# Kernel optimization log

Hardware: AMD Instinct MI355X
Metric: run time of the kernel (lower is better)

The kernel has to match this reference:

```python
import jax, jax.numpy as jnp
import numpy as np

MAX_RADIUS = 3.0
NUM_BASIS = 8
NUM_NEIGHBORS = 16.0
N, E, NS, NV, B, D, T, L, HR = 2048, 32768, 32, 16, 8, 32, 32, 2, 64
NW = NS * 2 * NV + NV * 2 * (NS + NV) + NV * 2 * NV  # 3072 per-edge TP weights


def smooth_cutoff(x):
    u = 2.0 * (x - 1.0)
    y = 0.5 * (1.0 - jnp.cos(jnp.pi * u))
    y = jnp.where(u > 0, 0.0, y)
    y = jnp.where(u < -1, 1.0, y)
    return y


def bessel_basis(length):
    # soft_one_hot_linspace(basis='bessel', cutoff=False) * sqrt(NUM_BASIS)
    k = jnp.arange(1, NUM_BASIS + 1, dtype=length.dtype) * jnp.pi
    l = jnp.maximum(length, 1e-9)[..., None]
    return jnp.sqrt(2.0 / MAX_RADIUS) * jnp.sin(k * l / MAX_RADIUS) / l * np.sqrt(NUM_BASIS)


def get_edge_info(x, edge_src, edge_dst):
    n = x.shape[0]
    xr = x.reshape(n, 2, 3)                         # 2 vectors per node
    vec = xr[edge_src] - xr[edge_dst]               # [E,2,3]
    length = jnp.sqrt(jnp.sum(vec * vec, axis=-1) + 1e-12)   # [E,2]
    sh = np.sqrt(3.0) * vec / length[..., None]     # component-normalized l=1 SH
    feat = bessel_basis(length)                     # [E,2,B]
    attr = smooth_cutoff(length / MAX_RADIUS)[..., None] * sh  # [E,2,3]
    return feat.reshape(vec.shape[0], -1), attr


def setup_inputs() -> dict:
    key = jax.random.key(0)
    ks = jax.random.split(key, 20)
    inp = {
        'x': jax.random.normal(ks[0], (N, 6), jnp.float32),
        'batch': jnp.zeros((N,), jnp.int64 if jax.config.jax_enable_x64 else jnp.int32),
        'node_attr': jax.random.randint(ks[1], (N,), 0, T),
        'edge_src': jax.random.randint(ks[2], (E,), 0, N),
        'edge_dst': jax.random.randint(ks[3], (E,), 0, N),
        'emb': jax.random.normal(ks[4], (T, D), jnp.float32),
        'W_uplift': jax.random.normal(ks[5], (NV, 2), jnp.float32),
        'W_sc_s': jax.random.normal(ks[6], (L, NS, D, NS + NV), jnp.float32),
        'W_sc_v': jax.random.normal(ks[7], (L, NV, D, NV), jnp.float32),
        'W_l1_s': jax.random.normal(ks[8], (L, NS, NS), jnp.float32),
        'W_l1_v': jax.random.normal(ks[9], (L, NV, NV), jnp.float32),
        'W_r1': jax.random.normal(ks[10], (L, 2 * B, HR), jnp.float32),
        'W_r2': jax.random.normal(ks[11], (L, HR, NW), jnp.float32),
        'W_l2_s': jax.random.normal(ks[12], (L, NS + NV, NS + NV), jnp.float32),
        'W_l2_v': jax.random.normal(ks[13], (L, NV, NV), jnp.float32),
        'W_si_s': jax.random.normal(ks[14], (L, NS, NS), jnp.float32),
        'W_si_v': jax.random.normal(ks[15], (L, NV, NV), jnp.float32),
        'h': jnp.ones((L,), jnp.float32) * 0.01,
        'mix': jnp.ones((L,), jnp.float32) * 0.5,
    }
    return inp


def reference(x, batch, node_attr, edge_src, edge_dst, emb, W_uplift, W_sc_s, W_sc_v,
              W_l1_s, W_l1_v, W_r1, W_r2, W_l2_s, W_l2_v, W_si_s, W_si_v, h, mix):
    n = x.shape[0]
    a = emb[node_attr]                              # node attr embedding [N,D]
    Q, _ = jnp.linalg.qr(W_uplift)                  # semi-unitary uplift [NV,2]
    y_v = jnp.einsum('ci,nik->nck', Q, x.reshape(n, 2, 3))   # uplift vectors
    y_s = jnp.zeros((n, NS), x.dtype)
    y, y_old = (y_s, y_v), (y_s, y_v)
    n1 = NS * 2 * NV
    n2 = NV * 2 * (NS + NV)
    for i in range(L):
        ef, ea = get_edge_info(x, edge_src, edge_dst)       # [E,2B], [E,2,3]
        ys, yv = y
        # self-connection tensor product (features x node_attr)
        sc_s = jnp.einsum('ni,na,iaj->nj', ys, a, W_sc_s[i]) / np.sqrt(NS * D)
        sc_v = jnp.einsum('nck,na,caj->njk', yv, a, W_sc_v[i]) / np.sqrt(NV * D)
        # lin1
        s1 = ys @ W_l1_s[i] / np.sqrt(NS)
        v1 = jnp.einsum('nck,cj->njk', yv, W_l1_v[i]) / np.sqrt(NV)
        # radial MLP -> per-edge TP weights
        hr = jax.nn.silu(ef @ W_r1[i] / np.sqrt(2 * B))
        w = hr @ W_r2[i] / np.sqrt(HR)                       # [E,NW]
        w_sv = w[:, :n1].reshape(E, NS, 2, NV)
        w_vs = w[:, n1:n1 + n2].reshape(E, NV, 2, NS + NV)
        w_vv = w[:, n1 + n2:].reshape(E, NV, 2, NV)
        s_src, v_src = s1[edge_src], v1[edge_src]
        # edge tensor product: 0e x 1o -> 1o, 1o x 1o -> 0e (dot), 1o x 1o -> 1o (cross)
        e_v = jnp.einsum('esmj,es,emk->ejk', w_sv, s_src, ea) / np.sqrt(NS * 2)
        dots = jnp.einsum('eck,emk->ecm', v_src, ea)
        e_s = jnp.einsum('ecmj,ecm->ej', w_vs, dots) / np.sqrt(NV * 2 * 3)
        crs = jnp.cross(v_src[:, :, None, :], ea[:, None, :, :])  # [E,NV,2,3]
        e_v = e_v + jnp.einsum('ecmj,ecmk->ejk', w_vv, crs) / np.sqrt(NV * 2 * 2)
        # scatter-aggregate over destination nodes
        ns_ = jax.ops.segment_sum(e_s, edge_dst, num_segments=n) / np.sqrt(NUM_NEIGHBORS)
        nv_ = jax.ops.segment_sum(e_v, edge_dst, num_segments=n) / np.sqrt(NUM_NEIGHBORS)
        s2 = ns_ @ W_l2_s[i] / np.sqrt(NS + NV)
        v2 = jnp.einsum('nck,cj->njk', nv_, W_l2_v[i]) / np.sqrt(NV)
        conv_s, conv_v = sc_s + s2, sc_v + v2
        # gate
        g_s = jax.nn.silu(conv_s[:, :NS])
        g_v = jax.nn.sigmoid(conv_s[:, NS:])[:, :, None] * conv_v
        # self-interaction
        si_s = ys @ W_si_s[i] / np.sqrt(NS)
        si_v = jnp.einsum('nck,cj->njk', yv, W_si_v[i]) / np.sqrt(NV)
        # gated leapfrog update
        h2, m = h[i] ** 2, mix[i]
        new_s = 2 * ys - y_old[0] + h2 * (m * g_s + (m - 1) * si_s)
        new_v = 2 * yv - y_old[1] + h2 * (m * g_v + (m - 1) * si_v)
        y_old, y = y, (new_s, new_v)
        x = jnp.einsum('ci,nck->nik', Q, y[1]).reshape(n, 6)  # project back
    return x
```

## Files before the change

### kernel.cpp

```cpp
#include <hip/hip_runtime.h>
#include <hip/hip_bf16.h>
#include <math.h>

#define NN   2048
#define EE   32768
#define NS   32
#define NV   16
#define NB   8
#define DD   32
#define TT   32
#define LL   2
#define HRD  64
#define NWW  3072
#define TPE  128
#define PI_F 3.14159265358979323846f

#define SC_SCS (1.0f/32.0f)
#define SC_SCV 0.04419417382415922f
#define SC_L1S 0.17677669529663687f
#define SC_L1V 0.25f
#define SC_R1  0.25f
#define SC_R2  0.125f
#define SC_ES  0.10206207261596575f
#define SC_EV  0.125f
#define SC_AGG 0.25f
#define SC_L2S 0.14433756729740643f
#define SC_L2V 0.25f
#define SC_SIS 0.17677669529663687f
#define SC_SIV 0.25f

typedef __attribute__((ext_vector_type(8))) short  short8;
typedef __attribute__((ext_vector_type(4))) float  floatx4;

__device__ __forceinline__ floatx4 mfma16(short8 a, short8 b, floatx4 c) {
    return __builtin_amdgcn_mfma_f32_16x16x32_bf16(a, b, c, 0, 0, 0);
}

__device__ __forceinline__ void seg_reduce_store(
        const float (*red)[49], const int* dst_s,
        const int* __restrict__ row_ptr, int ebase,
        int tid, int wave, int lane,
        int* segstart_s, int* wtot_s, int* nseg_s,
        float* __restrict__ outg) {
    int seg_flag = 0, seg_lidx = 0;
    if (tid < TPE) {
        seg_flag = (tid == 0) || (dst_s[tid] != dst_s[tid - 1]);
        unsigned long long m = __ballot(seg_flag != 0);
        if (lane == 0) wtot_s[wave] = (int)__popcll(m);
        seg_lidx = (int)__popcll(m & ((1ull << lane) - 1ull));
    }
    __syncthreads();
    if (seg_flag) segstart_s[seg_lidx + (wave ? wtot_s[0] : 0)] = tid;
    if (tid == 0) {
        int ns = wtot_s[0] + wtot_s[1];
        nseg_s[0] = ns;
        segstart_s[ns] = TPE;
    }
    __syncthreads();
    int nseg = nseg_s[0];
    for (int w = tid; w < nseg * 48; w += 256) {
        int seg = w / 48, c = w - seg * 48;
        int p0 = segstart_s[seg], p1 = segstart_s[seg + 1];
        int d = dst_s[p0];
        float run = 0.f;
        for (int pos = p0; pos < p1; ++pos) run += red[pos][c];
        if (row_ptr[d] >= ebase && row_ptr[d + 1] <= ebase + TPE)
            outg[d * 48 + c] = run;
        else
            atomicAdd(&outg[d * 48 + c], run);
    }
}

__global__ void k_setup(const float* __restrict__ Wup, float* __restrict__ Q,
                        const float* __restrict__ emb,
                        const float* __restrict__ Wscs, const float* __restrict__ Wscv,
                        float* __restrict__ WtS, float* __restrict__ WtV,
                        const float* __restrict__ Wr2, __hip_bfloat16* __restrict__ wr2t,
                        int* __restrict__ deg, int* __restrict__ cursor) {
    int b = blockIdx.x;
    if (b == 0) {
        if (threadIdx.x != 0) return;
        double A[16][2], tau[2];
        for (int i = 0; i < 16; ++i)
            for (int j = 0; j < 2; ++j) A[i][j] = (double)Wup[i*2 + j];
        for (int j = 0; j < 2; ++j) {
            double alpha = A[j][j];
            double xn2 = 0.0;
            for (int i = j + 1; i < 16; ++i) xn2 += A[i][j]*A[i][j];
            if (xn2 == 0.0) {
                tau[j] = 0.0;
            } else {
                double nrm  = sqrt(alpha*alpha + xn2);
                double beta = (alpha >= 0.0) ? -nrm : nrm;
                tau[j] = (beta - alpha) / beta;
                double s = 1.0 / (alpha - beta);
                for (int i = j + 1; i < 16; ++i) A[i][j] *= s;
                A[j][j] = beta;
            }
            for (int k = j + 1; k < 2; ++k) {
                double w = A[j][k];
                for (int i = j + 1; i < 16; ++i) w += A[i][j]*A[i][k];
                w *= tau[j];
                A[j][k] -= w;
                for (int i = j + 1; i < 16; ++i) A[i][k] -= A[i][j]*w;
            }
        }
        double Qm[16][2];
        for (int i = 0; i < 16; ++i)
            for (int j = 0; j < 2; ++j) Qm[i][j] = (i == j) ? 1.0 : 0.0;
        for (int j = 1; j >= 0; --j) {
            for (int k = 0; k < 2; ++k) {
                double w = Qm[j][k];
                for (int i = j + 1; i < 16; ++i) w += A[i][j]*Qm[i][k];
                w *= tau[j];
                Qm[j][k] -= w;
                for (int i = j + 1; i < 16; ++i) Qm[i][k] -= A[i][j]*w;
            }
        }
        for (int i = 0; i < 16; ++i)
            for (int j = 0; j < 2; ++j) Q[i*2 + j] = (float)Qm[i][j];
    } else if (b <= 64) {
        int lt = b - 1;
        int l = lt >> 5, t = lt & 31;
        __shared__ float es[32];
        if (threadIdx.x < 32) es[threadIdx.x] = emb[t*DD + threadIdx.x];
        __syncthreads();
        const float* Ws = Wscs + (size_t)l*NS*DD*48;
        float* oS = WtS + (size_t)(l*TT + t)*NS*48;
        for (int idx = threadIdx.x; idx < NS*48; idx += 256) {
            int i = idx / 48, j = idx % 48;
            float acc = 0.f;
            for (int a = 0; a < 32; ++a) acc += es[a]*Ws[(i*DD + a)*48 + j];
            oS[idx] = acc;
        }
        const float* Wv = Wscv + (size_t)l*NV*DD*NV;
        float* oV = WtV + (size_t)(l*TT + t)*NV*NV;
        for (int idx = threadIdx.x; idx < NV*NV; idx += 256) {
            int c = idx / 16, j = idx % 16;
            float acc = 0.f;
            for (int a = 0; a < 32; ++a) acc += es[a]*Wv[(c*DD + a)*NV + j];
            oV[idx] = acc;
        }
    } else if (b <= 1600) {
        int idx = (b - 65)*256 + threadIdx.x;
        int l = idx / (HRD*NWW);
        int r = idx - l*(HRD*NWW);
        int k = r / NWW;
        int c = r - k*NWW;
        int ch = c >> 6, cc = c & 63, q = cc >> 4, tcc = cc & 15;
        int h = k >> 5, qd = (k >> 3) & 3, j = k & 7;
        size_t dst = (size_t)l*(NWW*HRD)
                   + (size_t)((ch*32 + q*8 + h*4 + qd)*128 + tcc*8 + j);
        wr2t[dst] = __float2bfloat16(Wr2[idx]);
    } else {
        int i = (b - 1601)*256 + threadIdx.x;
        if (i < NN) { deg[i] = 0; cursor[i] = 0; }
    }
}

__global__ void k_hist(const int* __restrict__ edst, int* __restrict__ deg) {
    int e = blockIdx.x*256 + threadIdx.x;
    atomicAdd(&deg[edst[e]], 1);
}

__global__ void k_scan(const int* __restrict__ deg, int* __restrict__ row_ptr) {
    __shared__ int part[256];
    __shared__ int psc[256];
    int t = threadIdx.x;
    int loc[8]; int s = 0;
    for (int k = 0; k < 8; ++k) { loc[k] = deg[t*8 + k]; s += loc[k]; }
    part[t] = s;
    __syncthreads();
    if (t == 0) { int run = 0; for (int i = 0; i < 256; ++i) { psc[i] = run; run += part[i]; } }
    __syncthreads();
    int off = psc[t];
    for (int k = 0; k < 8; ++k) { row_ptr[t*8 + k] = off; off += loc[k]; }
    if (t == 255) row_ptr[2048] = off;
}

__global__ void k_fill(const int* __restrict__ esrc, const int* __restrict__ edst,
                       const int* __restrict__ row_ptr, int* __restrict__ cursor,
                       int* __restrict__ srcs, int* __restrict__ dsts,
                       const float* __restrict__ xin, const float* __restrict__ Q,
                       float* __restrict__ ys0, float* __restrict__ yv0,
                       float* __restrict__ ys1, float* __restrict__ yv1,
                       float* __restrict__ xcur,
                       const float* __restrict__ Wl1v0,
                       float* __restrict__ s1, float* __restrict__ v1,
                       float* __restrict__ nsb, float* __restrict__ nsb2,
                       float* __restrict__ nvba, float* __restrict__ nvbb) {
    if (blockIdx.x < 128) {
        int e = blockIdx.x*256 + threadIdx.x;
        int d = edst[e];
        int pos = atomicAdd(&cursor[d], 1);
        int p = row_ptr[d] + pos;
        srcs[p] = esrc[e];
        dsts[p] = d;
    } else {
        int idx = (blockIdx.x - 128)*256 + threadIdx.x;
        int n = idx / 48, r = idx - 48*(idx / 48);
        int j = r/3, k = r - 3*j;
        float xk  = xin[n*6 + k];
        float xk3 = xin[n*6 + 3 + k];
        float yvv = Q[j*2 + 0]*xk + Q[j*2 + 1]*xk3;
        yv0[idx] = yvv;
        yv1[idx] = yvv;
        float a = 0.f;
        for (int c = 0; c < 16; ++c) {
            float yc = Q[c*2 + 0]*xk + Q[c*2 + 1]*xk3;
            a += yc*Wl1v0[c*16 + j];
        }
        v1[idx] = a*SC_L1V;
        nsb[idx] = 0.f; nsb2[idx] = 0.f;
        nvba[idx] = 0.f; nvbb[idx] = 0.f;
        if (r < 32) {
            int si = n*32 + r;
            ys0[si] = 0.f; ys1[si] = 0.f; s1[si] = 0.f;
        }
        if (r < 6) xcur[n*6 + r] = xin[n*6 + r];
    }
}

__global__ void __launch_bounds__(256, 3) k_tp(
        const float* __restrict__ xcur,
        const int* __restrict__ srcs, const int* __restrict__ dsts,
        const int* __restrict__ row_ptr,
        const float* __restrict__ Wr1l,
        const __hip_bfloat16* __restrict__ wr2tl,
        const float* __restrict__ s1g, const float* __restrict__ v1g,
        float* __restrict__ nsb, float* __restrict__ nsb2,
        float* __restrict__ nvba, float* __restrict__ nvbb) {
    __shared__ __align__(16) char smem[42240];
    __shared__ float ea_s[TPE][9];
    __shared__ int   src_s[TPE];
    __shared__ int   dst_s[TPE];
    __shared__ int   segstart_s[TPE + 1];
    __shared__ int   wtot_s[2];
    __shared__ int   nseg_s[1];

    int bid = blockIdx.x;
    int region = bid % 3;
    int tile   = bid / 3;
    int ebase  = tile*TPE;
    int tid = threadIdx.x;
    int wave = tid >> 6, lane = tid & 63;
    int tc = tid & 15;
    int quad = lane >> 4;

    float* ef_lds  = (float*)smem;
    float* Wr1_lds = (float*)(smem + 8448);
    __hip_bfloat16* hr_lds = (__hip_bfloat16*)(smem + 12544);

    if (tid < TPE) { src_s[tid] = srcs[ebase + tid]; dst_s[tid] = dsts[ebase + tid]; }
    for (int i = tid; i < 16*64; i += 256) Wr1_lds[i] = Wr1l[i];

    if (tid < TPE) {
        int s = src_s[tid], d = dst_s[tid];
        for (int m = 0; m < 2; ++m) {
            float v0 = xcur[s*6 + m*3 + 0] - xcur[d*6 + m*3 + 0];
            float v1_ = xcur[s*6 + m*3 + 1] - xcur[d*6 + m*3 + 1];
            float v2 = xcur[s*6 + m*3 + 2] - xcur[d*6 + m*3 + 2];
            float len = sqrtf(v0*v0 + v1_*v1_ + v2*v2 + 1e-12f);
            float inv = 1.0f/len;
            float theta = len*(PI_F/3.0f);
            float s1v = sinf(theta), c1v = cosf(theta);
            float sc  = 2.3094010767585034f*inv;
            float sp = 0.f, scur = s1v, twoc = 2.f*c1v;
            for (int bq = 0; bq < 8; ++bq) {
                ef_lds[(m*8 + bq)*132 + tid] = sc*scur;
                float sn = twoc*scur - sp;
                sp = scur; scur = sn;
            }
            float u = 2.0f*(len*(1.0f/3.0f) - 1.0f);
            float cut;
            if (u > 0.f) cut = 0.f;
            else if (u < -1.f) cut = 1.f;
            else cut = 0.5f*(1.0f - cosf(PI_F*u));
            float shs = 1.7320508075688772f*inv*cut;
            ea_s[tid][m*3 + 0] = shs*v0;
            ea_s[tid][m*3 + 1] = shs*v1_;
            ea_s[tid][m*3 + 2] = shs*v2;
        }
    }
    __syncthreads();

    {
        int e = tid >> 1, h = tid & 1;
        float z[32];
        #pragma unroll
        for (int k = 0; k < 32; ++k) z[k] = 0.f;
        for (int f = 0; f < 16; ++f) {
            float efv = ef_lds[f*132 + e];
            #pragma unroll
            for (int k = 0; k < 32; ++k) z[k] += efv*Wr1_lds[f*64 + h*32 + k];
        }
        #pragma unroll
        for (int q8 = 0; q8 < 4; ++q8) {
            __hip_bfloat16 tmp[8];
            #pragma unroll
            for (int j = 0; j < 8; ++j) {
                float zz = z[q8*8 + j]*SC_R1;
                tmp[j] = __float2bfloat16(zz/(1.0f + expf(-zz)));
            }
            *(short8*)&hr_lds[e*72 + h*32 + q8*8] = *(short8*)tmp;
        }
    }
    __syncthreads();

    const short* hrp = (const short*)(smem + 12544);
    short8 a_lo[2], a_hi[2];
    #pragma unroll
    for (int rt = 0; rt < 2; ++rt) {
        int row = (wave*2 + rt)*16 + tc;
        a_lo[rt] = *(const short8*)(hrp + row*72 + quad*8);
        a_hi[rt] = *(const short8*)(hrp + row*72 + 32 + quad*8);
    }
    __syncthreads();

    const char* wb = (const char*)wr2tl;
    const float sES = SC_R2*SC_ES*SC_AGG;
    const float sEV = SC_R2*SC_EV*SC_AGG;

    if (region == 0) {
        float (*s1t)[132] = (float(*)[132])smem;
        for (int i = tid; i < TPE*32; i += 256) {
            int e = i >> 5, s = i & 31;
            s1t[s][e] = s1g[src_s[e]*32 + s];
        }
        __syncthreads();

        float accF[2][4][2] = {};
        for (int ci = 0; ci < 16; ++ci) {
            const char* Bc = wb + (size_t)ci*8192 + lane*16;
            #pragma unroll
            for (int q = 0; q < 4; ++q) {
                short8 b_lo = *(const short8*)(Bc + q*2048);
                short8 b_hi = *(const short8*)(Bc + q*2048 + 1024);
                floatx4 c0 = {0.f,0.f,0.f,0.f}, c1 = {0.f,0.f,0.f,0.f};
                c0 = mfma16(a_lo[0], b_lo, c0); c0 = mfma16(a_hi[0], b_hi, c0);
                c1 = mfma16(a_lo[1], b_lo, c1); c1 = mfma16(a_hi[1], b_hi, c1);
                int m = q & 1;
                int sidx = ci*2 + (q >> 1);
                #pragma unroll
                for (int rt = 0; rt < 2; ++rt) {
                    int e0r = (wave*2 + rt)*16 + quad*4;
                    float4 sv = *(const float4*)&s1t[sidx][e0r];
                    floatx4 cc = rt ? c1 : c0;
                    #pragma unroll
                    for (int i = 0; i < 4; ++i)
                        accF[rt][i][m] += cc[i]*((&sv.x)[i]);
                }
            }
        }
        __syncthreads();
        float (*red)[49] = (float(*)[49])smem;
        #pragma unroll
        for (int rt = 0; rt < 2; ++rt) {
            int e0r = (wave*2 + rt)*16 + quad*4;
            #pragma unroll
            for (int i = 0; i < 4; ++i) {
                int pos = e0r + i;
                float f0 = accF[rt][i][0]*sEV, f1 = accF[rt][i][1]*sEV;
                #pragma unroll
                for (int k = 0; k < 3; ++k)
                    red[pos][tc*3 + k] = f0*ea_s[pos][k] + f1*ea_s[pos][3 + k];
            }
        }
        __syncthreads();
        seg_reduce_store((const float(*)[49])smem, dst_s, row_ptr, ebase,
                         tid, wave, lane, segstart_s, wtot_s, nseg_s, nvba);
    } else if (region == 1) {
        float (*dots_t)[132] = (float(*)[132])smem;
        float (*v1t)[132]    = (float(*)[132])(smem + 16896);
        for (int i = tid; i < TPE*48; i += 256) {
            int e = i/48, j = i%48;
            v1t[j][e] = v1g[src_s[e]*48 + j];
        }
        __syncthreads();
        for (int i = tid; i < TPE*32; i += 256) {
            int cm = i >> 7, e = i & (TPE - 1), c = cm >> 1, m = cm & 1;
            dots_t[cm][e] = v1t[c*3+0][e]*ea_s[e][m*3+0]
                          + v1t[c*3+1][e]*ea_s[e][m*3+1]
                          + v1t[c*3+2][e]*ea_s[e][m*3+2];
        }
        __syncthreads();

        float accES[2][4][3] = {};
        for (int ci = 16; ci < 32; ++ci) {
            const char* Bc = wb + (size_t)ci*8192 + lane*16;
            #pragma unroll
            for (int q = 0; q < 4; ++q) {
                short8 b_lo = *(const short8*)(Bc + q*2048);
                short8 b_hi = *(const short8*)(Bc + q*2048 + 1024);
                floatx4 c0 = {0.f,0.f,0.f,0.f}, c1 = {0.f,0.f,0.f,0.f};
                c0 = mfma16(a_lo[0], b_lo, c0); c0 = mfma16(a_hi[0], b_hi, c0);
                c1 = mfma16(a_lo[1], b_lo, c1); c1 = mfma16(a_hi[1], b_hi, c1);
                int u = ci*4 + q - 64;
                int c = (u*10923) >> 16;
                int v6 = u - 6*c;
                int m = (v6 >= 3) ? 1 : 0;
                int g = v6 - 3*m;
                #pragma unroll
                for (int rt = 0; rt < 2; ++rt) {
                    int e0r = (wave*2 + rt)*16 + quad*4;
                    float4 dv = *(const float4*)&dots_t[c*2 + m][e0r];
                    floatx4 cc = rt ? c1 : c0;
                    #pragma unroll
                    for (int i = 0; i < 4; ++i)
                        accES[rt][i][g] += cc[i]*((&dv.x)[i]);
                }
            }
        }
        __syncthreads();
        float (*red)[49] = (float(*)[49])smem;
        #pragma unroll
        for (int rt = 0; rt < 2; ++rt) {
            int e0r = (wave*2 + rt)*16 + quad*4;
            #pragma unroll
            for (int i = 0; i < 4; ++i) {
                int pos = e0r + i;
                red[pos][tc]      = accES[rt][i][0]*sES;
                red[pos][16 + tc] = accES[rt][i][1]*sES;
                red[pos][32 + tc] = accES[rt][i][2]*sES;
            }
        }
        __syncthreads();
        seg_reduce_store((const float(*)[49])smem, dst_s, row_ptr, ebase,
                         tid, wave, lane, segstart_s, wtot_s, nseg_s, nsb);
    } else {
        float (*v1t)[132]  = (float(*)[132])smem;
        float (*dots2)[132] = (float(*)[132])(smem + 25344);
        for (int i = tid; i < TPE*48; i += 256) {
            int e = i/48, j = i%48;
            v1t[j][e] = v1g[src_s[e]*48 + j];
        }
        __syncthreads();
        for (int i = tid; i < 12*TPE; i += 256) {
            int r = i >> 7, e = i & (TPE - 1);
            int c = 10 + (r >> 1), m = r & 1;
            dots2[r][e] = v1t[c*3+0][e]*ea_s[e][m*3+0]
                        + v1t[c*3+1][e]*ea_s[e][m*3+1]
                        + v1t[c*3+2][e]*ea_s[e][m*3+2];
        }
        __syncthreads();

        float accES[2][4][3] = {};
        float accV[2][4][2][3] = {};
        for (int ci = 32; ci < 48; ++ci) {
            const char* Bc = wb + (size_t)ci*8192 + lane*16;
            #pragma unroll
            for (int q = 0; q < 4; ++q) {
                short8 b_lo = *(const short8*)(Bc + q*2048);
                short8 b_hi = *(const short8*)(Bc + q*2048 + 1024);
                floatx4 c0 = {0.f,0.f,0.f,0.f}, c1 = {0.f,0.f,0.f,0.f};
                c0 = mfma16(a_lo[0], b_lo, c0); c0 = mfma16(a_hi[0], b_hi, c0);
                c1 = mfma16(a_lo[1], b_lo, c1); c1 = mfma16(a_hi[1], b_hi, c1);
                if (ci < 40) {
                    int u = ci*4 + q - 64;
                    int c = (u*10923) >> 16;
                    int v6 = u - 6*c;
                    int m = (v6 >= 3) ? 1 : 0;
                    int g = v6 - 3*m;
                    int dr = (c - 10)*2 + m;
                    #pragma unroll
                    for (int rt = 0; rt < 2; ++rt) {
                        int e0r = (wave*2 + rt)*16 + quad*4;
                        float4 dv = *(const float4*)&dots2[dr][e0r];
                        floatx4 cc = rt ? c1 : c0;
                        #pragma unroll
                        for (int i = 0; i < 4; ++i)
                            accES[rt][i][g] += cc[i]*((&dv.x)[i]);
                    }
                } else {
                    int c = ci*2 - 80 + (q >> 1);
                    int m = q & 1;
                    #pragma unroll
                    for (int rt = 0; rt < 2; ++rt) {
                        int e0r = (wave*2 + rt)*16 + quad*4;
                        float4 vx = *(const float4*)&v1t[c*3 + 0][e0r];
                        float4 vy = *(const float4*)&v1t[c*3 + 1][e0r];
                        float4 vz = *(const float4*)&v1t[c*3 + 2][e0r];
                        floatx4 cc = rt ? c1 : c0;
                        #pragma unroll
                        for (int i = 0; i < 4; ++i) {
                            float ww = cc[i];
                            accV[rt][i][m][0] += ww*((&vx.x)[i]);
                            accV[rt][i][m][1] += ww*((&vy.x)[i]);
                            accV[rt][i][m][2] += ww*((&vz.x)[i]);
                        }
                    }
                }
            }
        }
        __syncthreads();
        float (*red)[49] = (float(*)[49])smem;
        #pragma unroll
        for (int rt = 0; rt < 2; ++rt) {
            int e0r = (wave*2 + rt)*16 + quad*4;
            #pragma unroll
            for (int i = 0; i < 4; ++i) {
                int pos = e0r + i;
                red[pos][tc]      = accES[rt][i][0]*sES;
                red[pos][16 + tc] = accES[rt][i][1]*sES;
                red[pos][32 + tc] = accES[rt][i][2]*sES;
            }
        }
        __syncthreads();
        seg_reduce_store((const float(*)[49])smem, dst_s, row_ptr, ebase,
                         tid, wave, lane, segstart_s, wtot_s, nseg_s, nsb2);
        __syncthreads();
        #pragma unroll
        for (int rt = 0; rt < 2; ++rt) {
            int e0r = (wave*2 + rt)*16 + quad*4;
            #pragma unroll
            for (int i = 0; i < 4; ++i) {
                int pos = e0r + i;
                float u00 = accV[rt][i][0][0], u01 = accV[rt][i][0][1], u02 = accV[rt][i][0][2];
                float u10 = accV[rt][i][1][0], u11 = accV[rt][i][1][1], u12 = accV[rt][i][1][2];
                float a0 = ea_s[pos][0], a1 = ea_s[pos][1], a2 = ea_s[pos][2];
                float b0 = ea_s[pos][3], b1 = ea_s[pos][4], b2 = ea_s[pos][5];
                red[pos][tc*3 + 0] = (u01*a2 - u02*a1 + u11*b2 - u12*b1)*sEV;
                red[pos][tc*3 + 1] = (u02*a0 - u00*a2 + u12*b0 - u10*b2)*sEV;
                red[pos][tc*3 + 2] = (u00*a1 - u01*a0 + u10*b1 - u11*b0)*sEV;
            }
        }
        __syncthreads();
        seg_reduce_store((const float(*)[49])smem, dst_s, row_ptr, ebase,
                         tid, wave, lane, segstart_s, wtot_s, nseg_s, nvbb);
    }
}

__global__ void __launch_bounds__(256) k_nodepost(
        const float* __restrict__ ysC, const float* __restrict__ yvC,
        float* __restrict__ ysO, float* __restrict__ yvO,
        const float* __restrict__ nsb, const float* __restrict__ nsb2,
        const float* __restrict__ nvba, const float* __restrict__ nvbb,
        const int* __restrict__ nattr,
        const float* __restrict__ WtSl, const float* __restrict__ WtVl,
        const float* __restrict__ Wl2s, const float* __restrict__ Wl2v,
        const float* __restrict__ Wsis, const float* __restrict__ Wsiv,
        const float* __restrict__ harr, const float* __restrict__ mixarr, int l,
        float* __restrict__ xcur, float* __restrict__ xout2,
        const float* __restrict__ Qg,
        const float* __restrict__ Wl1sN, const float* __restrict__ Wl1vN,
        float* __restrict__ s1, float* __restrict__ v1,
        float* __restrict__ znsb, float* __restrict__ znsb2,
        float* __restrict__ znvba, float* __restrict__ znvbb,
        int do_next) {
    int wave = threadIdx.x >> 6, lane = threadIdx.x & 63;
    int n = blockIdx.x*4 + wave;
    __shared__ float ys_s[4][32], yv_s[4][48], ns_s[4][48], nv_s[4][48];
    __shared__ float cs_s[4][48], nvo_s[4][48], nsn_s[4][32];

    if (lane < 32) ys_s[wave][lane] = ysC[n*32 + lane];
    if (lane < 48) {
        yv_s[wave][lane] = yvC[n*48 + lane];
        ns_s[wave][lane] = nsb[n*48 + lane] + nsb2[n*48 + lane];
        nv_s[wave][lane] = nvba[n*48 + lane] + nvbb[n*48 + lane];
    }
    __syncthreads();
    int t = nattr[n];
    const float* WtSn = WtSl + (size_t)t*NS*48;
    const float* WtVn = WtVl + (size_t)t*NV*NV;
    float hv = harr[l];
    float h2 = hv*hv, mx = mixarr[l];

    if (lane < 48) {
        float sc = 0.f, s2 = 0.f;
        for (int i = 0; i < 32; ++i) sc += ys_s[wave][i]*WtSn[i*48 + lane];
        for (int c = 0; c < 48; ++c) s2 += ns_s[wave][c]*Wl2s[c*48 + lane];
        cs_s[wave][lane] = sc*SC_SCS + s2*SC_L2S;
    }
    __syncthreads();
    if (lane < 48) {
        int j = lane/3, k = lane - 3*j;
        float scv = 0.f, v2 = 0.f, siv = 0.f;
        for (int c = 0; c < 16; ++c) {
            float yvv = yv_s[wave][c*3 + k];
            scv += yvv*WtVn[c*16 + j];
            v2  += nv_s[wave][c*3 + k]*Wl2v[c*16 + j];
            siv += yvv*Wsiv[c*16 + j];
        }
        float convv = scv*SC_SCV + v2*SC_L2V;
        siv *= SC_SIV;
        float gate = 1.f/(1.f + expf(-cs_s[wave][32 + j]));
        float gv = gate*convv;
        float nvnew = 2.f*yv_s[wave][lane] - yvO[n*48 + lane] + h2*(mx*gv + (mx - 1.f)*siv);
        nvo_s[wave][lane] = nvnew;
        yvO[n*48 + lane] = nvnew;
    }
    if (lane < 32) {
        float sis = 0.f;
        for (int i = 0; i < 32; ++i) sis += ys_s[wave][i]*Wsis[i*32 + lane];
        sis *= SC_SIS;
        float cs = cs_s[wave][lane];
        float gs = cs/(1.f + expf(-cs));
        float nsnew = 2.f*ys_s[wave][lane] - ysO[n*32 + lane] + h2*(mx*gs + (mx - 1.f)*sis);
        nsn_s[wave][lane] = nsnew;
        ysO[n*32 + lane] = nsnew;
    }
    __syncthreads();
    if (lane < 6) {
        int i = lane/3, k = lane - 3*(lane/3);
        float acc = 0.f;
        for (int c = 0; c < 16; ++c) acc += Qg[c*2 + i]*nvo_s[wave][c*3 + k];
        xcur[n*6 + lane]  = acc;
        xout2[n*6 + lane] = acc;
    }
    if (do_next) {
        if (lane < 32) {
            float a = 0.f;
            for (int i = 0; i < 32; ++i) a += nsn_s[wave][i]*Wl1sN[i*32 + lane];
            s1[n*32 + lane] = a*SC_L1S;
        }
        if (lane < 48) {
            int j = lane/3, k = lane - 3*j;
            float a = 0.f;
            for (int c = 0; c < 16; ++c) a += nvo_s[wave][c*3 + k]*Wl1vN[c*16 + j];
            v1[n*48 + lane] = a*SC_L1V;
            znsb[n*48 + lane] = 0.f; znsb2[n*48 + lane] = 0.f;
            znvba[n*48 + lane] = 0.f; znvbb[n*48 + lane] = 0.f;
        }
    }
}

extern "C" void kernel_launch(void* const* d_in, const int* in_sizes, int n_in,
                              void* d_out, int out_size, void* d_ws, size_t ws_size,
                              hipStream_t stream) {
    const float* x_in  = (const float*)d_in[0];
    const int*   nattr = (const int*)  d_in[2];
    const int*   esrc  = (const int*)  d_in[3];
    const int*   edst  = (const int*)  d_in[4];
    const float* emb   = (const float*)d_in[5];
    const float* Wup   = (const float*)d_in[6];
    const float* Wscs  = (const float*)d_in[7];
    const float* Wscv  = (const float*)d_in[8];
    const float* Wl1s  = (const float*)d_in[9];
    const float* Wl1v  = (const float*)d_in[10];
    const float* Wr1   = (const float*)d_in[11];
    const float* Wr2   = (const float*)d_in[12];
    const float* Wl2s  = (const float*)d_in[13];
    const float* Wl2v  = (const float*)d_in[14];
    const float* Wsis  = (const float*)d_in[15];
    const float* Wsiv  = (const float*)d_in[16];
    const float* harr  = (const float*)d_in[17];
    const float* mixar = (const float*)d_in[18];
    float* out = (float*)d_out;

    float* ws = (float*)d_ws;
    size_t off = 0;
    float* Q    = ws + off; off += 32;
    float* WtS  = ws + off; off += (size_t)LL*TT*NS*48;
    float* WtV  = ws + off; off += (size_t)LL*TT*NV*NV;
    float* ys0  = ws + off; off += (size_t)NN*32;
    float* yv0  = ws + off; off += (size_t)NN*48;
    float* ys1  = ws + off; off += (size_t)NN*32;
    float* yv1  = ws + off; off += (size_t)NN*48;
    float* xcur = ws + off; off += (size_t)NN*6;
    float* s1   = ws + off; off += (size_t)NN*32;
    float* v1   = ws + off; off += (size_t)NN*48;
    float* nsb  = ws + off; off += (size_t)NN*48;
    float* nsb2 = ws + off; off += (size_t)NN*48;
    float* nvba = ws + off; off += (size_t)NN*48;
    float* nvbb = ws + off; off += (size_t)NN*48;
    off = (off + 3) & ~(size_t)3;
    __hip_bfloat16* wr2t = (__hip_bfloat16*)(ws + off); off += (size_t)LL*NWW*HRD/2;
    int* deg     = (int*)(ws + off); off += NN;
    int* cursor  = (int*)(ws + off); off += NN;
    int* row_ptr = (int*)(ws + off); off += NN + 1;
    int* srcs    = (int*)(ws + off); off += EE;
    int* dsts    = (int*)(ws + off); off += EE;

    k_setup<<<1609, 256, 0, stream>>>(Wup, Q, emb, Wscs, Wscv, WtS, WtV, Wr2, wr2t,
                                      deg, cursor);
    k_hist<<<EE/256, 256, 0, stream>>>(edst, deg);
    k_scan<<<1, 256, 0, stream>>>(deg, row_ptr);
    k_fill<<<128 + NN*48/256, 256, 0, stream>>>(esrc, edst, row_ptr, cursor, srcs, dsts,
                                    x_in, Q, ys0, yv0, ys1, yv1, xcur,
                                    Wl1v, s1, v1, nsb, nsb2, nvba, nvbb);

    float* curS = ys0; float* curV = yv0;
    float* oldS = ys1; float* oldV = yv1;
    for (int l = 0; l < LL; ++l) {
        k_tp<<<3*EE/TPE, 256, 0, stream>>>(xcur, srcs, dsts, row_ptr,
                                           Wr1 + (size_t)l*16*64,
                                           wr2t + (size_t)l*NWW*HRD,
                                           s1, v1, nsb, nsb2, nvba, nvbb);
        float* xo2 = (l == LL - 1) ? out : xcur;
        int lN = (l + 1 < LL) ? (l + 1) : l;
        k_nodepost<<<NN/4, 256, 0, stream>>>(curS, curV, oldS, oldV,
                                             nsb, nsb2, nvba, nvbb, nattr,
                                             WtS + (size_t)l*TT*NS*48, WtV + (size_t)l*TT*NV*NV,
                                             Wl2s + (size_t)l*48*48, Wl2v + (size_t)l*16*16,
                                             Wsis + (size_t)l*32*32, Wsiv + (size_t)l*16*16,
                                             harr, mixar, l, xcur, xo2, Q,
                                             Wl1s + (size_t)lN*32*32, Wl1v + (size_t)lN*16*16,
                                             s1, v1, nsb, nsb2, nvba, nvbb,
                                             (l + 1 < LL) ? 1 : 0);
        float* ts = curS; curS = oldS; oldS = ts;
        float* tv = curV; curV = oldV; oldV = tv;
    }
}
```

Before: 232.4 us.

## Shrink tensor-product LDS footprint to raise occupancy; warp-shuffle scan for CSR

The region-1 staging of gathered v1 values now runs in two halves of 24 columns, which cuts the shared scratch buffer from 42240 to 31680 bytes. The launch bound is raised from 3 to 4 blocks per CU so more blocks can be resident and hide gather latency. This adds an extra round of barriers and may force register spilling under the tighter register budget. Separately, the single-thread serial prefix over 256 partial sums is replaced by a wavefront shuffle scan plus a small cross-wave combine.

```diff
diff --git a/kernel.cpp b/kernel.cpp
--- a/kernel.cpp
+++ b/kernel.cpp
@@ -164,16 +164,21 @@
 }
 
 __global__ void k_scan(const int* __restrict__ deg, int* __restrict__ row_ptr) {
-    __shared__ int part[256];
-    __shared__ int psc[256];
+    __shared__ int wsum[4];
     int t = threadIdx.x;
+    int lane = t & 63, wave = t >> 6;
     int loc[8]; int s = 0;
     for (int k = 0; k < 8; ++k) { loc[k] = deg[t*8 + k]; s += loc[k]; }
-    part[t] = s;
-    __syncthreads();
-    if (t == 0) { int run = 0; for (int i = 0; i < 256; ++i) { psc[i] = run; run += part[i]; } }
-    __syncthreads();
-    int off = psc[t];
+    int inc = s;
+    for (int d = 1; d < 64; d <<= 1) {
+        int v = __shfl_up(inc, d);
+        if (lane >= d) inc += v;
+    }
+    if (lane == 63) wsum[wave] = inc;
+    __syncthreads();
+    int woff = 0;
+    for (int w = 0; w < wave; ++w) woff += wsum[w];
+    int off = woff + inc - s;
     for (int k = 0; k < 8; ++k) { row_ptr[t*8 + k] = off; off += loc[k]; }
     if (t == 255) row_ptr[2048] = off;
 }
@@ -221,7 +226,7 @@
     }
 }
 
-__global__ void __launch_bounds__(256, 3) k_tp(
+__global__ void __launch_bounds__(256, 4) k_tp(
         const float* __restrict__ xcur,
         const int* __restrict__ srcs, const int* __restrict__ dsts,
         const int* __restrict__ row_ptr,
@@ -230,7 +235,7 @@
         const float* __restrict__ s1g, const float* __restrict__ v1g,
         float* __restrict__ nsb, float* __restrict__ nsb2,
         float* __restrict__ nvba, float* __restrict__ nvbb) {
-    __shared__ __align__(16) char smem[42240];
+    __shared__ __align__(16) char smem[31680];
     __shared__ float ea_s[TPE][9];
     __shared__ int   src_s[TPE];
     __shared__ int   dst_s[TPE];
@@ -371,19 +376,23 @@
                          tid, wave, lane, segstart_s, wtot_s, nseg_s, nvba);
     } else if (region == 1) {
         float (*dots_t)[132] = (float(*)[132])smem;
-        float (*v1t)[132]    = (float(*)[132])(smem + 16896);
-        for (int i = tid; i < TPE*48; i += 256) {
-            int e = i/48, j = i%48;
-            v1t[j][e] = v1g[src_s[e]*48 + j];
-        }
-        __syncthreads();
-        for (int i = tid; i < TPE*32; i += 256) {
-            int cm = i >> 7, e = i & (TPE - 1), c = cm >> 1, m = cm & 1;
-            dots_t[cm][e] = v1t[c*3+0][e]*ea_s[e][m*3+0]
-                          + v1t[c*3+1][e]*ea_s[e][m*3+1]
-                          + v1t[c*3+2][e]*ea_s[e][m*3+2];
-        }
-        __syncthreads();
+        float (*v1h)[132]    = (float(*)[132])(smem + 16896);
+        for (int half = 0; half < 2; ++half) {
+            int jbase = half*24;
+            for (int i = tid; i < TPE*24; i += 256) {
+                int e = i/24, j = i - 24*(i/24);
+                v1h[j][e] = v1g[src_s[e]*48 + jbase + j];
+            }
+            __syncthreads();
+            for (int i = tid; i < TPE*16; i += 256) {
+                int cm = i >> 7, e = i & (TPE - 1);
+                int c = cm >> 1, m = cm & 1;
+                dots_t[half*16 + cm][e] = v1h[c*3+0][e]*ea_s[e][m*3+0]
+                                        + v1h[c*3+1][e]*ea_s[e][m*3+1]
+                                        + v1h[c*3+2][e]*ea_s[e][m*3+2];
+            }
+            __syncthreads();
+        }
 
         float accES[2][4][3] = {};
         for (int ci = 16; ci < 32; ++ci) {
```

Result: slower. 281.1 us (+21.0%).

## Halve edge tile to 64 per block and use wave-shuffle scan

Applied to the files above, without the earlier changes.

Shrinks the per-block edge tile in the tensor-product kernel from 128 to 64 edges. That doubles the grid and halves LDS use, and each wave now handles one 16-row MFMA tile instead of two. The segment reduction drops to a single-wave ballot, and the prefix-scan kernel swaps its serial thread-0 loop for a shuffle-based wave scan. The aim is more blocks and occupancy to hide latency, at the cost of reloading the bf16 weight B-fragments from global memory twice as often and doing more boundary atomics.

```diff
diff --git a/kernel.cpp b/kernel.cpp
--- a/kernel.cpp
+++ b/kernel.cpp
@@ -12,7 +12,7 @@
 #define LL   2
 #define HRD  64
 #define NWW  3072
-#define TPE  128
+#define TPE  64
 #define PI_F 3.14159265358979323846f
 
 #define SC_SCS (1.0f/32.0f)
@@ -39,22 +39,20 @@
 __device__ __forceinline__ void seg_reduce_store(
         const float (*red)[49], const int* dst_s,
         const int* __restrict__ row_ptr, int ebase,
-        int tid, int wave, int lane,
+        int tid, int lane,
         int* segstart_s, int* wtot_s, int* nseg_s,
         float* __restrict__ outg) {
-    int seg_flag = 0, seg_lidx = 0;
     if (tid < TPE) {
-        seg_flag = (tid == 0) || (dst_s[tid] != dst_s[tid - 1]);
+        int seg_flag = (tid == 0) || (dst_s[tid] != dst_s[tid - 1]);
         unsigned long long m = __ballot(seg_flag != 0);
-        if (lane == 0) wtot_s[wave] = (int)__popcll(m);
-        seg_lidx = (int)__popcll(m & ((1ull << lane) - 1ull));
-    }
-    __syncthreads();
-    if (seg_flag) segstart_s[seg_lidx + (wave ? wtot_s[0] : 0)] = tid;
+        if (lane == 0) wtot_s[0] = (int)__popcll(m);
+        int seg_lidx = (int)__popcll(m & ((1ull << lane) - 1ull));
+        if (seg_flag) segstart_s[seg_lidx] = tid;
+    }
+    __syncthreads();
     if (tid == 0) {
-        int ns = wtot_s[0] + wtot_s[1];
-        nseg_s[0] = ns;
-        segstart_s[ns] = TPE;
+        nseg_s[0] = wtot_s[0];
+        segstart_s[wtot_s[0]] = TPE;
     }
     __syncthreads();
     int nseg = nseg_s[0];
@@ -164,16 +162,21 @@
 }
 
 __global__ void k_scan(const int* __restrict__ deg, int* __restrict__ row_ptr) {
-    __shared__ int part[256];
-    __shared__ int psc[256];
+    __shared__ int wsum[4];
     int t = threadIdx.x;
+    int lane = t & 63, wave = t >> 6;
     int loc[8]; int s = 0;
     for (int k = 0; k < 8; ++k) { loc[k] = deg[t*8 + k]; s += loc[k]; }
-    part[t] = s;
-    __syncthreads();
-    if (t == 0) { int run = 0; for (int i = 0; i < 256; ++i) { psc[i] = run; run += part[i]; } }
-    __syncthreads();
-    int off = psc[t];
+    int inc = s;
+    for (int d = 1; d < 64; d <<= 1) {
+        int v = __shfl_up(inc, d);
+        if (lane >= d) inc += v;
+    }
+    if (lane == 63) wsum[wave] = inc;
+    __syncthreads();
+    int woff = 0;
+    for (int w = 0; w < wave; ++w) woff += wsum[w];
+    int off = woff + inc - s;
     for (int k = 0; k < 8; ++k) { row_ptr[t*8 + k] = off; off += loc[k]; }
     if (t == 255) row_ptr[2048] = off;
 }
@@ -230,12 +233,12 @@
         const float* __restrict__ s1g, const float* __restrict__ v1g,
         float* __restrict__ nsb, float* __restrict__ nsb2,
         float* __restrict__ nvba, float* __restrict__ nvbb) {
-    __shared__ __align__(16) char smem[42240];
+    __shared__ __align__(16) char smem[21760];
     __shared__ float ea_s[TPE][9];
     __shared__ int   src_s[TPE];
     __shared__ int   dst_s[TPE];
     __shared__ int   segstart_s[TPE + 1];
-    __shared__ int   wtot_s[2];
+    __shared__ int   wtot_s[1];
     __shared__ int   nseg_s[1];
 
     int bid = blockIdx.x;
@@ -248,8 +251,8 @@
     int quad = lane >> 4;
 
     float* ef_lds  = (float*)smem;
-    float* Wr1_lds = (float*)(smem + 8448);
-    __hip_bfloat16* hr_lds = (__hip_bfloat16*)(smem + 12544);
+    float* Wr1_lds = (float*)(smem + 4352);
+    __hip_bfloat16* hr_lds = (__hip_bfloat16*)(smem + 8448);
 
     if (tid < TPE) { src_s[tid] = srcs[ebase + tid]; dst_s[tid] = dsts[ebase + tid]; }
     for (int i = tid; i < 16*64; i += 256) Wr1_lds[i] = Wr1l[i];
@@ -267,7 +270,7 @@
             float sc  = 2.3094010767585034f*inv;
             float sp = 0.f, scur = s1v, twoc = 2.f*c1v;
             for (int bq = 0; bq < 8; ++bq) {
-                ef_lds[(m*8 + bq)*132 + tid] = sc*scur;
+                ef_lds[(m*8 + bq)*68 + tid] = sc*scur;
                 float sn = twoc*scur - sp;
                 sp = scur; scur = sn;
             }
@@ -285,158 +288,135 @@
     __syncthreads();
 
     {
-        int e = tid >> 1, h = tid & 1;
-        float z[32];
+        int e = tid >> 2, h = tid & 3;
+        float z[16];
         #pragma unroll
-        for (int k = 0; k < 32; ++k) z[k] = 0.f;
+        for (int k = 0; k < 16; ++k) z[k] = 0.f;
         for (int f = 0; f < 16; ++f) {
-            float efv = ef_lds[f*132 + e];
+            float efv = ef_lds[f*68 + e];
             #pragma unroll
-            for (int k = 0; k < 32; ++k) z[k] += efv*Wr1_lds[f*64 + h*32 + k];
+            for (int k = 0; k < 16; ++k) z[k] += efv*Wr1_lds[f*64 + h*16 + k];
         }
         #pragma unroll
-        for (int q8 = 0; q8 < 4; ++q8) {
+        for (int q8 = 0; q8 < 2; ++q8) {
             __hip_bfloat16 tmp[8];
             #pragma unroll
             for (int j = 0; j < 8; ++j) {
                 float zz = z[q8*8 + j]*SC_R1;
                 tmp[j] = __float2bfloat16(zz/(1.0f + expf(-zz)));
             }
-            *(short8*)&hr_lds[e*72 + h*32 + q8*8] = *(short8*)tmp;
-        }
-    }
-    __syncthreads();
-
-    const short* hrp = (const short*)(smem + 12544);
-    short8 a_lo[2], a_hi[2];
-    #pragma unroll
-    for (int rt = 0; rt < 2; ++rt) {
-        int row = (wave*2 + rt)*16 + tc;
-        a_lo[rt] = *(const short8*)(hrp + row*72 + quad*8);
-        a_hi[rt] = *(const short8*)(hrp + row*72 + 32 + quad*8);
-    }
+            *(short8*)&hr_lds[e*72 + h*16 + q8*8] = *(short8*)tmp;
+        }
+    }
+    __syncthreads();
+
+    const short* hrp = (const short*)(smem + 8448);
+    int arow = wave*16 + tc;
+    short8 a_lo = *(const short8*)(hrp + arow*72 + quad*8);
+    short8 a_hi = *(const short8*)(hrp + arow*72 + 32 + quad*8);
     __syncthreads();
 
     const char* wb = (const char*)wr2tl;
     const float sES = SC_R2*SC_ES*SC_AGG;
     const float sEV = SC_R2*SC_EV*SC_AGG;
+    int e0r = wave*16 + quad*4;
 
     if (region == 0) {
-        float (*s1t)[132] = (float(*)[132])smem;
+        float (*s1t)[68] = (float(*)[68])smem;
         for (int i = tid; i < TPE*32; i += 256) {
             int e = i >> 5, s = i & 31;
             s1t[s][e] = s1g[src_s[e]*32 + s];
         }
         __syncthreads();
 
-        float accF[2][4][2] = {};
+        float accF[4][2] = {};
         for (int ci = 0; ci < 16; ++ci) {
             const char* Bc = wb + (size_t)ci*8192 + lane*16;
             #pragma unroll
             for (int q = 0; q < 4; ++q) {
                 short8 b_lo = *(const short8*)(Bc + q*2048);
                 short8 b_hi = *(const short8*)(Bc + q*2048 + 1024);
-                floatx4 c0 = {0.f,0.f,0.f,0.f}, c1 = {0.f,0.f,0.f,0.f};
-                c0 = mfma16(a_lo[0], b_lo, c0); c0 = mfma16(a_hi[0], b_hi, c0);
-                c1 = mfma16(a_lo[1], b_lo, c1); c1 = mfma16(a_hi[1], b_hi, c1);
+                floatx4 c0 = {0.f,0.f,0.f,0.f};
+                c0 = mfma16(a_lo, b_lo, c0); c0 = mfma16(a_hi, b_hi, c0);
                 int m = q & 1;
                 int sidx = ci*2 + (q >> 1);
+                float4 sv = *(const float4*)&s1t[sidx][e0r];
                 #pragma unroll
-                for (int rt = 0; rt < 2; ++rt) {
-                    int e0r = (wave*2 + rt)*16 + quad*4;
-                    float4 sv = *(const float4*)&s1t[sidx][e0r];
-                    floatx4 cc = rt ? c1 : c0;
-                    #pragma unroll
-                    for (int i = 0; i < 4; ++i)
-                        accF[rt][i][m] += cc[i]*((&sv.x)[i]);
-                }
+                for (int i = 0; i < 4; ++i)
+                    accF[i][m] += c0[i]*((&sv.x)[i]);
             }
         }
         __syncthreads();
         float (*red)[49] = (float(*)[49])smem;
         #pragma unroll
-        for (int rt = 0; rt < 2; ++rt) {
-            int e0r = (wave*2 + rt)*16 + quad*4;
+        for (int i = 0; i < 4; ++i) {
+            int pos = e0r + i;
+            float f0 = accF[i][0]*sEV, f1 = accF[i][1]*sEV;
             #pragma unroll
-            for (int i = 0; i < 4; ++i) {
-                int pos = e0r + i;
-                float f0 = accF[rt][i][0]*sEV, f1 = accF[rt][i][1]*sEV;
-                #pragma unroll
-                for (int k = 0; k < 3; ++k)
-                    red[pos][tc*3 + k] = f0*ea_s[pos][k] + f1*ea_s[pos][3 + k];
-            }
+            for (int k = 0; k < 3; ++k)
+                red[pos][tc*3 + k] = f0*ea_s[pos][k] + f1*ea_s[pos][3 + k];
         }
         __syncthreads();
         seg_reduce_store((const float(*)[49])smem, dst_s, row_ptr, ebase,
-                         tid, wave, lane, segstart_s, wtot_s, nseg_s, nvba);
+                         tid, lane, segstart_s, wtot_s, nseg_s, nvba);
     } else if (region == 1) {
-        float (*dots_t)[132] = (float(*)[132])smem;
-        float (*v1t)[132]    = (float(*)[132])(smem + 16896);
+        float (*dots_t)[68] = (float(*)[68])smem;
+        float (*v1t)[68]    = (float(*)[68])(smem + 8704);
         for (int i = tid; i < TPE*48; i += 256) {
-            int e = i/48, j = i%48;
+            int e = i/48, j = i - 48*(i/48);
             v1t[j][e] = v1g[src_s[e]*48 + j];
         }
         __syncthreads();
         for (int i = tid; i < TPE*32; i += 256) {
-            int cm = i >> 7, e = i & (TPE - 1), c = cm >> 1, m = cm & 1;
+            int cm = i >> 6, e = i & (TPE - 1), c = cm >> 1, m = cm & 1;
             dots_t[cm][e] = v1t[c*3+0][e]*ea_s[e][m*3+0]
                           + v1t[c*3+1][e]*ea_s[e][m*3+1]
                           + v1t[c*3+2][e]*ea_s[e][m*3+2];
         }
         __syncthreads();
 
-        float accES[2][4][3] = {};
+        float accES[4][3] = {};
         for (int ci = 16; ci < 32; ++ci) {
             const char* Bc = wb + (size_t)ci*8192 + lane*16;
             #pragma unroll
             for (int q = 0; q < 4; ++q) {
                 short8 b_lo = *(const short8*)(Bc + q*2048);
                 short8 b_hi = *(const short8*)(Bc + q*2048 + 1024);
-                floatx4 c0 = {0.f,0.f,0.f,0.f}, c1 = {0.f,0.f,0.f,0.f};
-                c0 = mfma16(a_lo[0], b_lo, c0); c0 = mfma16(a_hi[0], b_hi, c0);
-                c1 = mfma16(a_lo[1], b_lo, c1); c1 = mfma16(a_hi[1], b_hi, c1);
+                floatx4 c0 = {0.f,0.f,0.f,0.f};
+                c0 = mfma16(a_lo, b_lo, c0); c0 = mfma16(a_hi, b_hi, c0);
                 int u = ci*4 + q - 64;
                 int c = (u*10923) >> 16;
                 int v6 = u - 6*c;
                 int m = (v6 >= 3) ? 1 : 0;
                 int g = v6 - 3*m;
+                float4 dv = *(const float4*)&dots_t[c*2 + m][e0r];
                 #pragma unroll
-                for (int rt = 0; rt < 2; ++rt) {
-                    int e0r = (wave*2 + rt)*16 + quad*4;
-                    float4 dv = *(const float4*)&dots_t[c*2 + m][e0r];
-                    floatx4 cc = rt ? c1 : c0;
-                    #pragma unroll
-                    for (int i = 0; i < 4; ++i)
-                        accES[rt][i][g] += cc[i]*((&dv.x)[i]);
-                }
+                for (int i = 0; i < 4; ++i)
+                    accES[i][g] += c0[i]*((&dv.x)[i]);
             }
         }
         __syncthreads();
         float (*red)[49] = (float(*)[49])smem;
         #pragma unroll
-        for (int rt = 0; rt < 2; ++rt) {
-            int e0r = (wave*2 + rt)*16 + quad*4;
-            #pragma unroll
-            for (int i = 0; i < 4; ++i) {
-                int pos = e0r + i;
-                red[pos][tc]      = accES[rt][i][0]*sES;
-                red[pos][16 + tc] = accES[rt][i][1]*sES;
-                red[pos][32 + tc] = accES[rt][i][2]*sES;
-            }
+        for (int i = 0; i < 4; ++i) {
+            int pos = e0r + i;
+            red[pos][tc]      = accES[i][0]*sES;
+            red[pos][16 + tc] = accES[i][1]*sES;
+            red[pos][32 + tc] = accES[i][2]*sES;
         }
         __syncthreads();
         seg_reduce_store((const float(*)[49])smem, dst_s, row_ptr, ebase,
-                         tid, wave, lane, segstart_s, wtot_s, nseg_s, nsb);
+                         tid, lane, segstart_s, wtot_s, nseg_s, nsb);
     } else {
-        float (*v1t)[132]  = (float(*)[132])smem;
-        float (*dots2)[132] = (float(*)[132])(smem + 25344);
+        float (*v1t)[68]   = (float(*)[68])smem;
+        float (*dots2)[68] = (float(*)[68])(smem + 13056);
         for (int i = tid; i < TPE*48; i += 256) {
-            int e = i/48, j = i%48;
+            int e = i/48, j = i - 48*(i/48);
             v1t[j][e] = v1g[src_s[e]*48 + j];
         }
         __syncthreads();
         for (int i = tid; i < 12*TPE; i += 256) {
-            int r = i >> 7, e = i & (TPE - 1);
+            int r = i >> 6, e = i & (TPE - 1);
             int c = 10 + (r >> 1), m = r & 1;
             dots2[r][e] = v1t[c*3+0][e]*ea_s[e][m*3+0]
                         + v1t[c*3+1][e]*ea_s[e][m*3+1]
@@ -444,17 +424,16 @@
         }
         __syncthreads();
 
-        float accES[2][4][3] = {};
-        float accV[2][4][2][3] = {};
+        float accES[4][3] = {};
+        float accV[4][2][3] = {};
         for (int ci = 32; ci < 48; ++ci) {
             const char* Bc = wb + (size_t)ci*8192 + lane*16;
             #pragma unroll
             for (int q = 0; q < 4; ++q) {
                 short8 b_lo = *(const short8*)(Bc + q*2048);
                 short8 b_hi = *(const short8*)(Bc + q*2048 + 1024);
-                floatx4 c0 = {0.f,0.f,0.f,0.f}, c1 = {0.f,0.f,0.f,0.f};
-                c0 = mfma16(a_lo[0], b_lo, c0); c0 = mfma16(a_hi[0], b_hi, c0);
-                c1 = mfma16(a_lo[1], b_lo, c1); c1 = mfma16(a_hi[1], b_hi, c1);
+                floatx4 c0 = {0.f,0.f,0.f,0.f};
+                c0 = mfma16(a_lo, b_lo, c0); c0 = mfma16(a_hi, b_hi, c0);
                 if (ci < 40) {
                     int u = ci*4 + q - 64;
                     int c = (u*10923) >> 16;
@@ -462,32 +441,22 @@
                     int m = (v6 >= 3) ? 1 : 0;
                     int g = v6 - 3*m;
                     int dr = (c - 10)*2 + m;
+                    float4 dv = *(const float4*)&dots2[dr][e0r];
                     #pragma unroll
-                    for (int rt = 0; rt < 2; ++rt) {
-                        int e0r = (wave*2 + rt)*16 + quad*4;
-                        float4 dv = *(const float4*)&dots2[dr][e0r];
-                        floatx4 cc = rt ? c1 : c0;
-                        #pragma unroll
-                        for (int i = 0; i < 4; ++i)
-                            accES[rt][i][g] += cc[i]*((&dv.x)[i]);
-                    }
+                    for (int i = 0; i < 4; ++i)
+                        accES[i][g] += c0[i]*((&dv.x)[i]);
                 } else {
                     int c = ci*2 - 80 + (q >> 1);
                     int m = q & 1;
+                    float4 vx = *(const float4*)&v1t[c*3 + 0][e0r];
+                    float4 vy = *(const float4*)&v1t[c*3 + 1][e0r];
+                    float4 vz = *(const float4*)&v1t[c*3 + 2][e0r];
                     #pragma unroll
-                    for (int rt = 0; rt < 2; ++rt) {
-                        int e0r = (wave*2 + rt)*16 + quad*4;
-                        float4 vx = *(const float4*)&v1t[c*3 + 0][e0r];
-                        float4 vy = *(const float4*)&v1t[c*3 + 1][e0r];
-                        float4 vz = *(const float4*)&v1t[c*3 + 2][e0r];
-                        floatx4 cc = rt ? c1 : c0;
-                        #pragma unroll
-                        for (int i = 0; i < 4; ++i) {
-                            float ww = cc[i];
-                            accV[rt][i][m][0] += ww*((&vx.x)[i]);
-                            accV[rt][i][m][1] += ww*((&vy.x)[i]);
-                            accV[rt][i][m][2] += ww*((&vz.x)[i]);
-                        }
+                    for (int i = 0; i < 4; ++i) {
+                        float ww = c0[i];
+                        accV[i][m][0] += ww*((&vx.x)[i]);
+                        accV[i][m][1] += ww*((&vy.x)[i]);
+                        accV[i][m][2] += ww*((&vz.x)[i]);
                     }
                 }
             }
@@ -495,38 +464,30 @@
         __syncthreads();
         float (*red)[49] = (float(*)[49])smem;
         #pragma unroll
-        for (int rt = 0; rt < 2; ++rt) {
-            int e0r = (wave*2 + rt)*16 + quad*4;
-            #pragma unroll
-            for (int i = 0; i < 4; ++i) {
-                int pos = e0r + i;
-                red[pos][tc]      = accES[rt][i][0]*sES;
-                red[pos][16 + tc] = accES[rt][i][1]*sES;
-                red[pos][32 + tc] = accES[rt][i][2]*sES;
-            }
+        for (int i = 0; i < 4; ++i) {
+            int pos = e0r + i;
+            red[pos][tc]      = accES[i][0]*sES;
+            red[pos][16 + tc] = accES[i][1]*sES;
+            red[pos][32 + tc] = accES[i][2]*sES;
         }
         __syncthreads();
         seg_reduce_store((const float(*)[49])smem, dst_s, row_ptr, ebase,
-                         tid, wave, lane, segstart_s, wtot_s, nseg_s, nsb2);
+                         tid, lane, segstart_s, wtot_s, nseg_s, nsb2);
         __syncthreads();
         #pragma unroll
-        for (int rt = 0; rt < 2; ++rt) {
-            int e0r = (wave*2 + rt)*16 + quad*4;
-            #pragma unroll
-            for (int i = 0; i < 4; ++i) {
-                int pos = e0r + i;
-                float u00 = accV[rt][i][0][0], u01 = accV[rt][i][0][1], u02 = accV[rt][i][0][2];
-                float u10 = accV[rt][i][1][0], u11 = accV[rt][i][1][1], u12 = accV[rt][i][1][2];
-                float a0 = ea_s[pos][0], a1 = ea_s[pos][1], a2 = ea_s[pos][2];
-                float b0 = ea_s[pos][3], b1 = ea_s[pos][4], b2 = ea_s[pos][5];
-                red[pos][tc*3 + 0] = (u01*a2 - u02*a1 + u11*b2 - u12*b1)*sEV;
-                red[pos][tc*3 + 1] = (u02*a0 - u00*a2 + u12*b0 - u10*b2)*sEV;
-                red[pos][tc*3 + 2] = (u00*a1 - u01*a0 + u10*b1 - u11*b0)*sEV;
-            }
+        for (int i = 0; i < 4; ++i) {
+            int pos = e0r + i;
+            float u00 = accV[i][0][0], u01 = accV[i][0][1], u02 = accV[i][0][2];
+            float u10 = accV[i][1][0], u11 = accV[i][1][1], u12 = accV[i][1][2];
+            float a0 = ea_s[pos][0], a1 = ea_s[pos][1], a2 = ea_s[pos][2];
+            float b0 = ea_s[pos][3], b1 = ea_s[pos][4], b2 = ea_s[pos][5];
+            red[pos][tc*3 + 0] = (u01*a2 - u02*a1 + u11*b2 - u12*b1)*sEV;
+            red[pos][tc*3 + 1] = (u02*a0 - u00*a2 + u12*b0 - u10*b2)*sEV;
+            red[pos][tc*3 + 2] = (u00*a1 - u01*a0 + u10*b1 - u11*b0)*sEV;
         }
         __syncthreads();
         seg_reduce_store((const float(*)[49])smem, dst_s, row_ptr, ebase,
-                         tid, wave, lane, segstart_s, wtot_s, nseg_s, nvbb);
+                         tid, lane, segstart_s, wtot_s, nseg_s, nvbb);
     }
 }
 
```

New measurement: 354.3 us. +52.5%, slower.
